# Kernel optimization log

Hardware: AMD Instinct MI355X
Metric: run time of the kernel (lower is better)

The kernel has to match this reference:

```python
import jax, jax.numpy as jnp
import numpy as np

GRID_SIZE = 5
SPLINE_ORDER = 3
NUM_BASIS = GRID_SIZE + SPLINE_ORDER  # 8
BATCH = 4096
POINTS = 512
EMBD = 2048
IN0 = 2 * POINTS - 1  # 1023


def make_grid():
    # torch: arange(-k, G+k+1) * h + grid_range[0], h=(1-(-1))/G=0.4 -> 12 knots
    h = 2.0 / GRID_SIZE
    return jnp.arange(-SPLINE_ORDER, GRID_SIZE + SPLINE_ORDER + 1, dtype=jnp.float32) * h - 1.0


def b_splines(x, grid):
    # x: (N, F) -> bases: (N, F, NUM_BASIS) via Cox-de Boor recursion
    xg = x[..., None]
    bases = ((xg >= grid[:-1]) & (xg < grid[1:])).astype(x.dtype)
    for k in range(1, SPLINE_ORDER + 1):
        left = (xg - grid[:-(k + 1)]) / (grid[k:-1] - grid[:-(k + 1)])
        right = (grid[k + 1:] - xg) / (grid[k + 1:] - grid[1:-k])
        bases = left * bases[..., :-1] + right * bases[..., 1:]
    return bases


def kan_linear(x, base_w, spline_w, scaler, grid):
    # base path: ReLU(x) @ base_w^T  (base_activation=nn.ReLU in KAN)
    base_out = jax.nn.relu(x) @ base_w.T
    # spline path: b_splines(x) blended with scaled spline weights
    bases = b_splines(x, grid)                      # (N, F, K)
    sw = spline_w * scaler[..., None]               # (O, F, K)
    spline_out = jnp.einsum('nfk,ofk->no', bases, sw)
    return base_out + spline_out


def setup_inputs() -> dict:
    key = jax.random.key(0)
    ks = jax.random.split(key, 12)
    dims = [(IN0, EMBD), (EMBD, EMBD), (EMBD, POINTS)]
    inp = {
        'xs': jax.random.uniform(ks[0], (BATCH, POINTS, 1), dtype=jnp.float32),
        'ys': jax.random.uniform(ks[1], (BATCH, POINTS), dtype=jnp.float32),
    }
    i = 2
    for l, (fi, fo) in enumerate(dims):
        s = 1.0 / np.sqrt(fi)
        inp[f'base_w{l}'] = jax.random.normal(ks[i], (fo, fi), dtype=jnp.float32) * s
        inp[f'spline_w{l}'] = jax.random.normal(ks[i + 1], (fo, fi, NUM_BASIS), dtype=jnp.float32) * s
        inp[f'scaler{l}'] = jax.random.normal(ks[i + 2], (fo, fi), dtype=jnp.float32) * s
        i += 3
    return inp


def reference(xs, ys, base_w0, spline_w0, scaler0, base_w1, spline_w1, scaler1,
              base_w2, spline_w2, scaler2):
    grid = make_grid()
    xs2 = xs[:, :, 0]                               # (B, P)
    b = xs2.shape[0]
    # interleave x/y pairs, append final x: (B, 2P-1)
    inter = jnp.stack([xs2[:, :-1], ys[:, :-1]], axis=-1).reshape(b, -1)
    h = jnp.concatenate([inter, xs2[:, -1:]], axis=1)
    h = kan_linear(h, base_w0, spline_w0, scaler0, grid)
    h = kan_linear(h, base_w1, spline_w1, scaler1, grid)
    h = kan_linear(h, base_w2, spline_w2, scaler2, grid)
    return h
```

## Files before the change

### kernel.cpp

```cpp
#include <hip/hip_runtime.h>

#define GLOBAL_AS __attribute__((address_space(1)))
#define LDS_AS    __attribute__((address_space(3)))

typedef __bf16 bf16x8 __attribute__((ext_vector_type(8)));
typedef float  floatx4 __attribute__((ext_vector_type(4)));
typedef unsigned short ushort8 __attribute__((ext_vector_type(8)));

static constexpr int M_BATCH = 4096;
static constexpr int NPTS    = 512;
static constexpr int EMB     = 2048;
static constexpr int F0      = 1023;
static constexpr int F0P     = 1024;
static constexpr int K0      = 9 * F0P;
static constexpr int K12     = 9 * EMB;

__device__ __forceinline__ unsigned short f2bf(float f) {
    unsigned int u = __float_as_uint(f);
    u += 0x7fffu + ((u >> 16) & 1u);
    return (unsigned short)(u >> 16);
}

__device__ __forceinline__ void kan_phi(float x, float* v) {
    float b[11];
    #pragma unroll
    for (int i = 0; i < 11; ++i) {
        const float gl = (float)(i - 3) * 0.4f - 1.0f;
        const float gr = (float)(i - 2) * 0.4f - 1.0f;
        b[i] = (x >= gl && x < gr) ? 1.0f : 0.0f;
    }
    #pragma unroll
    for (int k = 1; k <= 3; ++k) {
        #pragma unroll
        for (int i = 0; i + k < 11; ++i) {
            const float gi   = (float)(i - 3) * 0.4f - 1.0f;
            const float gi1  = (float)(i - 2) * 0.4f - 1.0f;
            const float gik  = (float)(i + k - 3) * 0.4f - 1.0f;
            const float gik1 = (float)(i + k - 2) * 0.4f - 1.0f;
            const float invL = 1.0f / (gik - gi);
            const float invR = 1.0f / (gik1 - gi1);
            b[i] = (x - gi) * invL * b[i] + (gik1 - x) * invR * b[i + 1];
        }
    }
    v[0] = x > 0.0f ? x : 0.0f;
    #pragma unroll
    for (int i = 0; i < 8; ++i) v[1 + i] = b[i];
}

template<int FP, int MODE>
__global__ __launch_bounds__(256)
void aux2_kernel(const float* __restrict__ p0,
                 const float* __restrict__ p1,
                 unsigned short* __restrict__ phi,
                 int F, int NE,
                 const float* __restrict__ bw,
                 const float* __restrict__ sw,
                 const float* __restrict__ sc,
                 unsigned short* __restrict__ wt) {
    constexpr int RPB = (FP == 1024) ? 2 : 1;
    const int tid = threadIdx.x;
    const int u   = (RPB == 2) ? (tid & 127) : tid;
    const int f0  = u * 8;

    if ((int)blockIdx.x < NE) {
        const int n = blockIdx.x * RPB + (RPB == 2 ? (tid >> 7) : 0);
        float xv[8];
        if (MODE == 1) {
            const float4 xsv = *reinterpret_cast<const float4*>(p0 + (size_t)n * NPTS + (f0 >> 1));
            const float4 ysv = *reinterpret_cast<const float4*>(p1 + (size_t)n * NPTS + (f0 >> 1));
            xv[0] = xsv.x; xv[1] = ysv.x; xv[2] = xsv.y; xv[3] = ysv.y;
            xv[4] = xsv.z; xv[5] = ysv.z; xv[6] = xsv.w; xv[7] = ysv.w;
        } else {
            const float4 a0 = *reinterpret_cast<const float4*>(p0 + (size_t)n * F + f0);
            const float4 a1 = *reinterpret_cast<const float4*>(p0 + (size_t)n * F + f0 + 4);
            const float4 c0 = *reinterpret_cast<const float4*>(p1 + (size_t)n * F + f0);
            const float4 c1 = *reinterpret_cast<const float4*>(p1 + (size_t)n * F + f0 + 4);
            xv[0] = a0.x + c0.x; xv[1] = a0.y + c0.y; xv[2] = a0.z + c0.z; xv[3] = a0.w + c0.w;
            xv[4] = a1.x + c1.x; xv[5] = a1.y + c1.y; xv[6] = a1.z + c1.z; xv[7] = a1.w + c1.w;
        }
        ushort8 out[9];
        #pragma unroll
        for (int i = 0; i < 8; ++i) {
            float v[9];
            kan_phi(xv[i], v);
            const bool valid = (f0 + i) < F;
            #pragma unroll
            for (int s = 0; s < 9; ++s) {
                const int flat = i * 9 + s;
                out[flat >> 3][flat & 7] = valid ? f2bf(v[s]) : (unsigned short)0;
            }
        }
        ushort8* dst = reinterpret_cast<ushort8*>(phi + (size_t)n * (size_t)(9 * FP) + (size_t)f0 * 9);
        #pragma unroll
        for (int w = 0; w < 9; ++w) dst[w] = out[w];
    } else {
        const int o = (blockIdx.x - NE) * RPB + (RPB == 2 ? (tid >> 7) : 0);
        const float4* swr = reinterpret_cast<const float4*>(sw + ((size_t)o * F + f0) * 8);
        float scv[8], bwv[8];
        #pragma unroll
        for (int i = 0; i < 8; ++i) {
            const bool valid = (f0 + i) < F;
            scv[i] = valid ? sc[(size_t)o * F + f0 + i] : 0.0f;
            bwv[i] = valid ? bw[(size_t)o * F + f0 + i] : 0.0f;
        }
        ushort8 out[9];
        #pragma unroll
        for (int i = 0; i < 8; ++i) {
            const bool valid = (f0 + i) < F;
            float4 lo = float4{0.f, 0.f, 0.f, 0.f}, hi = float4{0.f, 0.f, 0.f, 0.f};
            if (valid) { lo = swr[i * 2]; hi = swr[i * 2 + 1]; }
            const float s = scv[i];
            float w9[9];
            w9[0] = bwv[i];
            w9[1] = lo.x * s; w9[2] = lo.y * s; w9[3] = lo.z * s; w9[4] = lo.w * s;
            w9[5] = hi.x * s; w9[6] = hi.y * s; w9[7] = hi.z * s; w9[8] = hi.w * s;
            #pragma unroll
            for (int s2 = 0; s2 < 9; ++s2) {
                const int flat = i * 9 + s2;
                out[flat >> 3][flat & 7] = valid ? f2bf(w9[s2]) : (unsigned short)0;
            }
        }
        ushort8* dst = reinterpret_cast<ushort8*>(wt + (size_t)o * (size_t)(9 * FP) + (size_t)f0 * 9);
        #pragma unroll
        for (int w = 0; w < 9; ++w) dst[w] = out[w];
    }
}

#define STAGE_H(GB, LB) do { \
    __builtin_amdgcn_global_load_lds((const GLOBAL_AS void*)((GB) + (size_t)r6 * K + scol), \
        (LDS_AS void*)((LB) + wv512), 16, 0, 0); \
    __builtin_amdgcn_global_load_lds((const GLOBAL_AS void*)((GB) + (size_t)(64 + r6) * K + scol), \
        (LDS_AS void*)((LB) + 4096 + wv512), 16, 0, 0); \
} while (0)

__global__ __launch_bounds__(512, 2)
void gemm_bt_256(const unsigned short* __restrict__ A,
                 const unsigned short* __restrict__ B,
                 float* __restrict__ C,
                 int M, int N, int K, int kchunk) {
    __shared__ __align__(16) unsigned short Alds[2 * 16384];
    __shared__ __align__(16) unsigned short Blds[2 * 16384];

    const int tid  = threadIdx.x;
    const int wv   = tid >> 6;
    const int lane = tid & 63;
    const int fr   = lane & 15;
    const int fq   = lane >> 4;
    const int wmi  = wv >> 2;
    const int wni  = wv & 3;

    const int bm = blockIdx.y;
    const int bn = blockIdx.x;
    const int kbase = blockIdx.z * kchunk;
    const int NT = kchunk >> 6;
    float* Cz = C + (size_t)blockIdx.z * (size_t)M * N;

    const int r6    = tid >> 3;
    const int scol  = ((tid & 7) ^ (r6 & 7)) * 8;
    const int wv512 = wv * 512;

    const unsigned short* Ab = A + (size_t)bm * 256 * K;
    const unsigned short* Bb = B + (size_t)bn * 256 * K;

    const int aoff0 = (wmi * 16 + fr) * 64 + ((fq    ) ^ (fr & 7)) * 8;
    const int aoff1 = (wmi * 16 + fr) * 64 + ((4 + fq) ^ (fr & 7)) * 8;
    const int boff0 = (wni * 16 + fr) * 64 + ((fq    ) ^ (fr & 7)) * 8;
    const int boff1 = (wni * 16 + fr) * 64 + ((4 + fq) ^ (fr & 7)) * 8;

    floatx4 zero = {0.f, 0.f, 0.f, 0.f};
    floatx4 acc[8][4];
    #pragma unroll
    for (int i = 0; i < 8; ++i)
        #pragma unroll
        for (int j = 0; j < 4; ++j)
            acc[i][j] = zero;

    {
        const unsigned short* Ag = Ab + kbase;
        const unsigned short* Bg = Bb + kbase;
        STAGE_H(Bg,                   Blds);
        STAGE_H(Ag,                   Alds);
        STAGE_H(Bg + (size_t)128 * K, Blds + 8192);
        STAGE_H(Ag + (size_t)128 * K, Alds + 8192);
        STAGE_H(Bg + 64,                   Blds + 16384);
        STAGE_H(Ag + 64,                   Alds + 16384);
        STAGE_H(Bg + (size_t)128 * K + 64, Blds + 16384 + 8192);
    }
    asm volatile("s_waitcnt vmcnt(6)" ::: "memory");
    __builtin_amdgcn_s_barrier();

    for (int t = 0; t < NT; ++t) {
        unsigned short* Ac = Alds + (t & 1) * 16384;
        unsigned short* Bc = Blds + (t & 1) * 16384;
        const int t1 = (t + 1 < NT) ? t + 1 : NT - 1;
        const int t2 = (t + 2 < NT) ? t + 2 : NT - 1;
        const unsigned short* Ag1 = Ab + kbase + t1 * 64;
        const unsigned short* Ag2 = Ab + kbase + t2 * 64;
        const unsigned short* Bg2 = Bb + kbase + t2 * 64;
        unsigned short* Al1 = Alds + (t1 & 1) * 16384;
        unsigned short* Al2 = Alds + (t2 & 1) * 16384;
        unsigned short* Bl2 = Blds + (t2 & 1) * 16384;

        bf16x8 a_lo[4][2], a_hi[4][2], b_lo[2][2], b_hi[2][2];

        #pragma unroll
        for (int mt = 0; mt < 4; ++mt) {
            a_lo[mt][0] = *reinterpret_cast<const bf16x8*>(Ac + mt * 2048 + aoff0);
            a_lo[mt][1] = *reinterpret_cast<const bf16x8*>(Ac + mt * 2048 + aoff1);
        }
        #pragma unroll
        for (int nt = 0; nt < 2; ++nt) {
            b_lo[nt][0] = *reinterpret_cast<const bf16x8*>(Bc + nt * 4096 + boff0);
            b_lo[nt][1] = *reinterpret_cast<const bf16x8*>(Bc + nt * 4096 + boff1);
        }
        STAGE_H(Ag1 + (size_t)128 * K, Al1 + 8192);
        __builtin_amdgcn_s_barrier();
        asm volatile("s_waitcnt lgkmcnt(0)" ::: "memory");
        __builtin_amdgcn_s_setprio(1);
        #pragma unroll
        for (int mt = 0; mt < 4; ++mt)
            #pragma unroll
            for (int nt = 0; nt < 2; ++nt) {
                acc[mt][nt] = __builtin_amdgcn_mfma_f32_16x16x32_bf16(a_lo[mt][0], b_lo[nt][0], acc[mt][nt], 0, 0, 0);
                acc[mt][nt] = __builtin_amdgcn_mfma_f32_16x16x32_bf16(a_lo[mt][1], b_lo[nt][1], acc[mt][nt], 0, 0, 0);
            }
        __builtin_amdgcn_s_setprio(0);
        __builtin_amdgcn_s_barrier();

        #pragma unroll
        for (int nt = 0; nt < 2; ++nt) {
            b_hi[nt][0] = *reinterpret_cast<const bf16x8*>(Bc + (2 + nt) * 4096 + boff0);
            b_hi[nt][1] = *reinterpret_cast<const bf16x8*>(Bc + (2 + nt) * 4096 + boff1);
        }
        STAGE_H(Bg2, Bl2);
        __builtin_amdgcn_s_barrier();
        asm volatile("s_waitcnt lgkmcnt(0)" ::: "memory");
        __builtin_amdgcn_s_setprio(1);
        #pragma unroll
        for (int mt = 0; mt < 4; ++mt)
            #pragma unroll
            for (int nt = 0; nt < 2; ++nt) {
                acc[mt][2 + nt] = __builtin_amdgcn_mfma_f32_16x16x32_bf16(a_lo[mt][0], b_hi[nt][0], acc[mt][2 + nt], 0, 0, 0);
                acc[mt][2 + nt] = __builtin_amdgcn_mfma_f32_16x16x32_bf16(a_lo[mt][1], b_hi[nt][1], acc[mt][2 + nt], 0, 0, 0);
            }
        __builtin_amdgcn_s_setprio(0);
        __builtin_amdgcn_s_barrier();

        #pragma unroll
        for (int mt = 0; mt < 4; ++mt) {
            a_hi[mt][0] = *reinterpret_cast<const bf16x8*>(Ac + (4 + mt) * 2048 + aoff0);
            a_hi[mt][1] = *reinterpret_cast<const bf16x8*>(Ac + (4 + mt) * 2048 + aoff1);
        }
        STAGE_H(Ag2, Al2);
        __builtin_amdgcn_s_barrier();
        asm volatile("s_waitcnt lgkmcnt(0)" ::: "memory");
        __builtin_amdgcn_s_setprio(1);
        #pragma unroll
        for (int mt = 0; mt < 4; ++mt)
            #pragma unroll
            for (int nt = 0; nt < 2; ++nt) {
                acc[4 + mt][nt] = __builtin_amdgcn_mfma_f32_16x16x32_bf16(a_hi[mt][0], b_lo[nt][0], acc[4 + mt][nt], 0, 0, 0);
                acc[4 + mt][nt] = __builtin_amdgcn_mfma_f32_16x16x32_bf16(a_hi[mt][1], b_lo[nt][1], acc[4 + mt][nt], 0, 0, 0);
            }
        __builtin_amdgcn_s_setprio(0);
        __builtin_amdgcn_s_barrier();

        STAGE_H(Bg2 + (size_t)128 * K, Bl2 + 8192);
        __builtin_amdgcn_s_barrier();
        __builtin_amdgcn_s_setprio(1);
        #pragma unroll
        for (int mt = 0; mt < 4; ++mt)
            #pragma unroll
            for (int nt = 0; nt < 2; ++nt) {
                acc[4 + mt][2 + nt] = __builtin_amdgcn_mfma_f32_16x16x32_bf16(a_hi[mt][0], b_hi[nt][0], acc[4 + mt][2 + nt], 0, 0, 0);
                acc[4 + mt][2 + nt] = __builtin_amdgcn_mfma_f32_16x16x32_bf16(a_hi[mt][1], b_hi[nt][1], acc[4 + mt][2 + nt], 0, 0, 0);
            }
        __builtin_amdgcn_s_setprio(0);
        asm volatile("s_waitcnt vmcnt(6)" ::: "memory");
        __builtin_amdgcn_s_barrier();
    }

    #pragma unroll
    for (int mt = 0; mt < 8; ++mt) {
        #pragma unroll
        for (int nt = 0; nt < 4; ++nt) {
            #pragma unroll
            for (int r = 0; r < 4; ++r) {
                int gr = bm * 256 + mt * 32 + wmi * 16 + fq * 4 + r;
                int gc = bn * 256 + nt * 64 + wni * 16 + fr;
                Cz[(size_t)gr * N + gc] = acc[mt][nt][r];
            }
        }
    }
}

__global__ void add8_kernel(const float* __restrict__ p,
                            float* __restrict__ out, int n4, int slice4) {
    int i = blockIdx.x * blockDim.x + threadIdx.x;
    if (i >= n4) return;
    const float4* p4 = reinterpret_cast<const float4*>(p);
    float4 s = p4[i];
    #pragma unroll
    for (int z = 1; z < 8; ++z) {
        float4 v = p4[(size_t)z * slice4 + i];
        s.x += v.x; s.y += v.y; s.z += v.z; s.w += v.w;
    }
    reinterpret_cast<float4*>(out)[i] = s;
}

extern "C" void kernel_launch(void* const* d_in, const int* in_sizes, int n_in,
                              void* d_out, int out_size, void* d_ws, size_t ws_size,
                              hipStream_t stream) {
    const float* xs  = (const float*)d_in[0];
    const float* ys  = (const float*)d_in[1];
    const float* bw0 = (const float*)d_in[2];
    const float* sw0 = (const float*)d_in[3];
    const float* sc0 = (const float*)d_in[4];
    const float* bw1 = (const float*)d_in[5];
    const float* sw1 = (const float*)d_in[6];
    const float* sc1 = (const float*)d_in[7];
    const float* bw2 = (const float*)d_in[8];
    const float* sw2 = (const float*)d_in[9];
    const float* sc2 = (const float*)d_in[10];

    char* ws = (char*)d_ws;
    unsigned short* Phi = (unsigned short*)ws;
    unsigned short* Wt  = (unsigned short*)(ws + 150994944);
    float* Cpart = (float*)(ws + 150994944 + 75497472);
    float* out = (float*)d_out;
    (void)ws_size; (void)in_sizes; (void)n_in; (void)out_size;

    const int T = 256;
    const size_t MN = (size_t)M_BATCH * EMB;

    aux2_kernel<F0P, 1><<<2048 + 1024, T, 0, stream>>>(
        xs, ys, Phi, F0, 2048, bw0, sw0, sc0, Wt);
    gemm_bt_256<<<dim3(8, 16, 2), 512, 0, stream>>>(Phi, Wt, Cpart, M_BATCH, EMB, K0, K0 / 2);

    aux2_kernel<EMB, 0><<<M_BATCH + EMB, T, 0, stream>>>(
        Cpart, Cpart + MN, Phi, EMB, M_BATCH, bw1, sw1, sc1, Wt);
    gemm_bt_256<<<dim3(8, 16, 2), 512, 0, stream>>>(Phi, Wt, Cpart, M_BATCH, EMB, K12, K12 / 2);

    aux2_kernel<EMB, 0><<<M_BATCH + NPTS, T, 0, stream>>>(
        Cpart, Cpart + MN, Phi, EMB, M_BATCH, bw2, sw2, sc2, Wt);
    gemm_bt_256<<<dim3(2, 16, 8), 512, 0, stream>>>(Phi, Wt, Cpart, M_BATCH, NPTS, K12, K12 / 8);
    add8_kernel<<<(M_BATCH * NPTS / 4 + T - 1) / T, T, 0, stream>>>(
        Cpart, out, M_BATCH * NPTS / 4, M_BATCH * NPTS / 4);
}
```

Before: 998.9 us.

## Stage phi and weight packing through LDS for coalesced global stores

The prep kernel now assigns one row per block and builds the packed 9-slot bf16 row in shared memory first. It then writes the row out with contiguous, fully coalesced 16-byte stores, and the weight side reads scaler, base and spline weights as coalesced float4 vectors. Before, each thread wrote nine strided 16-byte chunks and read spline weights with a large per-thread stride. The change trades more blocks (one row per block for layer 0) and extra LDS traffic plus syncs for better global access patterns. The LDS scatter writes of 2-byte elements may cause bank conflicts.

```diff
diff --git a/kernel.cpp b/kernel.cpp
--- a/kernel.cpp
+++ b/kernel.cpp
@@ -49,7 +49,7 @@
 
 template<int FP, int MODE>
 __global__ __launch_bounds__(256)
-void aux2_kernel(const float* __restrict__ p0,
+void aux3_kernel(const float* __restrict__ p0,
                  const float* __restrict__ p1,
                  unsigned short* __restrict__ phi,
                  int F, int NE,
@@ -57,72 +57,105 @@
                  const float* __restrict__ sw,
                  const float* __restrict__ sc,
                  unsigned short* __restrict__ wt) {
-    constexpr int RPB = (FP == 1024) ? 2 : 1;
-    const int tid = threadIdx.x;
-    const int u   = (RPB == 2) ? (tid & 127) : tid;
-    const int f0  = u * 8;
+    __shared__ __align__(16) unsigned short W[9 * FP];
+    __shared__ __align__(16) float scL[FP];
+    const int tid  = threadIdx.x;
+    const int NW8  = (9 * FP) / 8;
 
     if ((int)blockIdx.x < NE) {
-        const int n = blockIdx.x * RPB + (RPB == 2 ? (tid >> 7) : 0);
-        float xv[8];
+        const int n = blockIdx.x;
         if (MODE == 1) {
-            const float4 xsv = *reinterpret_cast<const float4*>(p0 + (size_t)n * NPTS + (f0 >> 1));
-            const float4 ysv = *reinterpret_cast<const float4*>(p1 + (size_t)n * NPTS + (f0 >> 1));
-            xv[0] = xsv.x; xv[1] = ysv.x; xv[2] = xsv.y; xv[3] = ysv.y;
-            xv[4] = xsv.z; xv[5] = ysv.z; xv[6] = xsv.w; xv[7] = ysv.w;
+            const int half = tid >> 7;
+            const int q    = tid & 127;
+            const float* src = half ? p1 : p0;
+            const float4 v = *reinterpret_cast<const float4*>(
+                src + (size_t)n * NPTS + (size_t)q * 4);
+            const float xv[4] = {v.x, v.y, v.z, v.w};
+            #pragma unroll
+            for (int c = 0; c < 4; ++c) {
+                const int f = 8 * q + 2 * c + half;
+                float ph[9];
+                kan_phi(xv[c], ph);
+                const bool valid = f < F;
+                #pragma unroll
+                for (int s = 0; s < 9; ++s)
+                    W[f * 9 + s] = valid ? f2bf(ph[s]) : (unsigned short)0;
+            }
         } else {
-            const float4 a0 = *reinterpret_cast<const float4*>(p0 + (size_t)n * F + f0);
-            const float4 a1 = *reinterpret_cast<const float4*>(p0 + (size_t)n * F + f0 + 4);
-            const float4 c0 = *reinterpret_cast<const float4*>(p1 + (size_t)n * F + f0);
-            const float4 c1 = *reinterpret_cast<const float4*>(p1 + (size_t)n * F + f0 + 4);
-            xv[0] = a0.x + c0.x; xv[1] = a0.y + c0.y; xv[2] = a0.z + c0.z; xv[3] = a0.w + c0.w;
-            xv[4] = a1.x + c1.x; xv[5] = a1.y + c1.y; xv[6] = a1.z + c1.z; xv[7] = a1.w + c1.w;
-        }
-        ushort8 out[9];
-        #pragma unroll
-        for (int i = 0; i < 8; ++i) {
-            float v[9];
-            kan_phi(xv[i], v);
-            const bool valid = (f0 + i) < F;
-            #pragma unroll
-            for (int s = 0; s < 9; ++s) {
-                const int flat = i * 9 + s;
-                out[flat >> 3][flat & 7] = valid ? f2bf(v[s]) : (unsigned short)0;
-            }
-        }
-        ushort8* dst = reinterpret_cast<ushort8*>(phi + (size_t)n * (size_t)(9 * FP) + (size_t)f0 * 9);
-        #pragma unroll
-        for (int w = 0; w < 9; ++w) dst[w] = out[w];
+            #pragma unroll
+            for (int r = 0; r < 2; ++r) {
+                const int q = tid + r * 256;
+                const float4 a = *reinterpret_cast<const float4*>(
+                    p0 + (size_t)n * F + (size_t)q * 4);
+                const float4 c4 = *reinterpret_cast<const float4*>(
+                    p1 + (size_t)n * F + (size_t)q * 4);
+                const float xv[4] = {a.x + c4.x, a.y + c4.y, a.z + c4.z, a.w + c4.w};
+                #pragma unroll
+                for (int c = 0; c < 4; ++c) {
+                    const int f = q * 4 + c;
+                    float ph[9];
+                    kan_phi(xv[c], ph);
+                    #pragma unroll
+                    for (int s = 0; s < 9; ++s)
+                        W[f * 9 + s] = f2bf(ph[s]);
+                }
+            }
+        }
+        __syncthreads();
+        ushort8* dst = reinterpret_cast<ushort8*>(phi + (size_t)n * (size_t)(9 * FP));
+        const ushort8* srcW = reinterpret_cast<const ushort8*>(W);
+        for (int idx = tid; idx < NW8; idx += 256) dst[idx] = srcW[idx];
     } else {
-        const int o = (blockIdx.x - NE) * RPB + (RPB == 2 ? (tid >> 7) : 0);
-        const float4* swr = reinterpret_cast<const float4*>(sw + ((size_t)o * F + f0) * 8);
-        float scv[8], bwv[8];
-        #pragma unroll
-        for (int i = 0; i < 8; ++i) {
-            const bool valid = (f0 + i) < F;
-            scv[i] = valid ? sc[(size_t)o * F + f0 + i] : 0.0f;
-            bwv[i] = valid ? bw[(size_t)o * F + f0 + i] : 0.0f;
-        }
-        ushort8 out[9];
-        #pragma unroll
-        for (int i = 0; i < 8; ++i) {
-            const bool valid = (f0 + i) < F;
-            float4 lo = float4{0.f, 0.f, 0.f, 0.f}, hi = float4{0.f, 0.f, 0.f, 0.f};
-            if (valid) { lo = swr[i * 2]; hi = swr[i * 2 + 1]; }
-            const float s = scv[i];
-            float w9[9];
-            w9[0] = bwv[i];
-            w9[1] = lo.x * s; w9[2] = lo.y * s; w9[3] = lo.z * s; w9[4] = lo.w * s;
-            w9[5] = hi.x * s; w9[6] = hi.y * s; w9[7] = hi.z * s; w9[8] = hi.w * s;
-            #pragma unroll
-            for (int s2 = 0; s2 < 9; ++s2) {
-                const int flat = i * 9 + s2;
-                out[flat >> 3][flat & 7] = valid ? f2bf(w9[s2]) : (unsigned short)0;
-            }
-        }
-        ushort8* dst = reinterpret_cast<ushort8*>(wt + (size_t)o * (size_t)(9 * FP) + (size_t)f0 * 9);
-        #pragma unroll
-        for (int w = 0; w < 9; ++w) dst[w] = out[w];
+        const int o = blockIdx.x - NE;
+        for (int i = tid; i < FP / 4; i += 256) {
+            float4 v;
+            if (i * 4 + 4 <= F) {
+                v = *reinterpret_cast<const float4*>(sc + (size_t)o * F + (size_t)i * 4);
+            } else {
+                float tmp[4];
+                #pragma unroll
+                for (int c = 0; c < 4; ++c)
+                    tmp[c] = (i * 4 + c < F) ? sc[(size_t)o * F + i * 4 + c] : 0.0f;
+                v = float4{tmp[0], tmp[1], tmp[2], tmp[3]};
+            }
+            *reinterpret_cast<float4*>(&scL[i * 4]) = v;
+        }
+        for (int i = tid; i < FP / 4; i += 256) {
+            float4 v;
+            if (i * 4 + 4 <= F) {
+                v = *reinterpret_cast<const float4*>(bw + (size_t)o * F + (size_t)i * 4);
+            } else {
+                float tmp[4];
+                #pragma unroll
+                for (int c = 0; c < 4; ++c)
+                    tmp[c] = (i * 4 + c < F) ? bw[(size_t)o * F + i * 4 + c] : 0.0f;
+                v = float4{tmp[0], tmp[1], tmp[2], tmp[3]};
+            }
+            const float vv[4] = {v.x, v.y, v.z, v.w};
+            #pragma unroll
+            for (int c = 0; c < 4; ++c) {
+                const int f = i * 4 + c;
+                W[f * 9] = (f < F) ? f2bf(vv[c]) : (unsigned short)0;
+            }
+        }
+        __syncthreads();
+        for (int i = tid; i < FP * 2; i += 256) {
+            const int f = i >> 1;
+            const int h = i & 1;
+            float4 v = float4{0.f, 0.f, 0.f, 0.f};
+            if (i < 2 * F)
+                v = *reinterpret_cast<const float4*>(
+                    sw + (size_t)o * F * 8 + (size_t)i * 4);
+            const float s = scL[f];
+            const float vv[4] = {v.x * s, v.y * s, v.z * s, v.w * s};
+            #pragma unroll
+            for (int c = 0; c < 4; ++c)
+                W[f * 9 + 1 + 4 * h + c] = (f < F) ? f2bf(vv[c]) : (unsigned short)0;
+        }
+        __syncthreads();
+        ushort8* dst = reinterpret_cast<ushort8*>(wt + (size_t)o * (size_t)(9 * FP));
+        const ushort8* srcW = reinterpret_cast<const ushort8*>(W);
+        for (int idx = tid; idx < NW8; idx += 256) dst[idx] = srcW[idx];
     }
 }
 
@@ -333,15 +366,15 @@
     const int T = 256;
     const size_t MN = (size_t)M_BATCH * EMB;
 
-    aux2_kernel<F0P, 1><<<2048 + 1024, T, 0, stream>>>(
-        xs, ys, Phi, F0, 2048, bw0, sw0, sc0, Wt);
+    aux3_kernel<F0P, 1><<<M_BATCH + EMB, T, 0, stream>>>(
+        xs, ys, Phi, F0, M_BATCH, bw0, sw0, sc0, Wt);
     gemm_bt_256<<<dim3(8, 16, 2), 512, 0, stream>>>(Phi, Wt, Cpart, M_BATCH, EMB, K0, K0 / 2);
 
-    aux2_kernel<EMB, 0><<<M_BATCH + EMB, T, 0, stream>>>(
+    aux3_kernel<EMB, 0><<<M_BATCH + EMB, T, 0, stream>>>(
         Cpart, Cpart + MN, Phi, EMB, M_BATCH, bw1, sw1, sc1, Wt);
     gemm_bt_256<<<dim3(8, 16, 2), 512, 0, stream>>>(Phi, Wt, Cpart, M_BATCH, EMB, K12, K12 / 2);
 
-    aux2_kernel<EMB, 0><<<M_BATCH + NPTS, T, 0, stream>>>(
+    aux3_kernel<EMB, 0><<<M_BATCH + NPTS, T, 0, stream>>>(
         Cpart, Cpart + MN, Phi, EMB, M_BATCH, bw2, sw2, sc2, Wt);
     gemm_bt_256<<<dim3(2, 16, 8), 512, 0, stream>>>(Phi, Wt, Cpart, M_BATCH, NPTS, K12, K12 / 8);
     add8_kernel<<<(M_BATCH * NPTS / 4 + T - 1) / T, T, 0, stream>>>(
```

Result: faster. 920.5 us (-7.8%).
